# Kernel tuning notes

Measured on AMD Instinct MI355X. Metric: run time of the kernel, lower is better.

Reference implementation:

```python
import jax, jax.numpy as jnp
import numpy as np

N_HEAD = 16
D_HEAD = 64
HIDDEN = 1024
T = 2048
B = 4


def setup_inputs() -> dict:
    key = jax.random.key(0)
    k1, k2, k3, k4, k5 = jax.random.split(key, 5)
    qkv_out = (2 * N_HEAD + 1) * D_HEAD  # 2112
    return {
        "x": jax.random.normal(k1, (B, T, HIDDEN), dtype=jnp.float32),
        "w_qkv": jax.random.normal(k2, (qkv_out, HIDDEN), dtype=jnp.float32) * (HIDDEN ** -0.5),
        "b_qkv": jax.random.normal(k3, (qkv_out,), dtype=jnp.float32) * 0.02,
        "w_out": jax.random.normal(k4, (HIDDEN, D_HEAD), dtype=jnp.float32) * (D_HEAD ** -0.5),
        "b_out": jax.random.normal(k5, (HIDDEN,), dtype=jnp.float32) * 0.02,
    }


def reference(x, w_qkv, b_qkv, w_out, b_out):
    bs, t, h = x.shape
    scale = D_HEAD ** -0.5
    qkv = x @ w_qkv.T + b_qkv  # [b, t, (2H+1)*dh]
    q, k, v = jnp.split(qkv, [N_HEAD * D_HEAD, 2 * N_HEAD * D_HEAD], axis=-1)
    q = q.reshape(bs, t, N_HEAD, D_HEAD)
    k = k.reshape(bs, t, N_HEAD, D_HEAD)
    v = v.reshape(bs, t, D_HEAD)  # single V head shared across all heads
    # attn_score: [b, h, i, j]
    attn_score = jnp.einsum("bihd,bjhd->bhij", q, k) * scale
    # causal mask: -inf above diagonal
    causal = jnp.triu(jnp.full((t, t), -jnp.inf, dtype=attn_score.dtype), 1)
    attn_score = attn_score + causal
    attn_prob = jax.nn.softmax(attn_score, axis=-1)  # dropout is identity in eval
    # shared V across heads: [b,h,i,j] x [b,j,d] -> [b,h,i,d]
    attn_vec = jnp.einsum("bhij,bjd->bhid", attn_prob, v)
    m_attn_vec = jnp.mean(attn_vec, axis=1)  # mean over heads -> [b, t, d_head]
    out = m_attn_vec @ w_out.T + b_out  # [b, t, hidden]
    return out, attn_vec
```

## Files before the change

### kernel.cpp

```cpp
#include <hip/hip_runtime.h>
#include <hip/hip_bf16.h>
#include <math.h>

#define NHEAD 16
#define DHEAD 64
#define HIDDEN 1024
#define TSEQ 2048
#define BATCH 4
#define QKV_OUT 2112
#define BT (BATCH * TSEQ)

typedef __attribute__((ext_vector_type(8))) short bf16x8;
typedef __attribute__((ext_vector_type(4))) float floatx4;

static __device__ __forceinline__ short f2bf(float x) {
  __hip_bfloat16 h = __float2bfloat16(x);
  return *reinterpret_cast<short*>(&h);
}

#define MFMA16(a, b, c) __builtin_amdgcn_mfma_f32_16x16x32_bf16(a, b, c, 0, 0, 0)

__global__ __launch_bounds__(256) void f32_to_bf16(
    const float* __restrict__ src, short* __restrict__ dst, int n) {
  const int i = (blockIdx.x * 256 + threadIdx.x) * 8;
  if (i >= n) return;
  float4 a = *(const float4*)&src[i];
  float4 b = *(const float4*)&src[i + 4];
  short o[8];
  o[0] = f2bf(a.x); o[1] = f2bf(a.y); o[2] = f2bf(a.z); o[3] = f2bf(a.w);
  o[4] = f2bf(b.x); o[5] = f2bf(b.y); o[6] = f2bf(b.z); o[7] = f2bf(b.w);
  *(uint4*)&dst[i] = *(uint4*)o;
}

#define QK_BM 128
#define QK_BN 64
#define QK_BK 64

template <typename OUT_T>
__global__ __launch_bounds__(256) void gemm_mfma_bf16(
    const short* __restrict__ A, const short* __restrict__ B,
    const float* __restrict__ bias, OUT_T* __restrict__ C,
    int M, int N, int K) {
  __shared__ short As[QK_BM][72];
  __shared__ short Bs[QK_BN][72];

  const int tid = threadIdx.x;
  const int lane = tid & 63;
  const int wv = tid >> 6;
  const int ln = lane & 15;
  const int grp = lane >> 4;
  const int wm = wv >> 1;
  const int wn = wv & 1;
  const int rowbase = blockIdx.y * QK_BM;
  const int colbase = blockIdx.x * QK_BN;

  const int ar = tid >> 1, ac = (tid & 1) * 32;
  const int br = tid >> 2, bc = (tid & 3) * 16;

  floatx4 acc[4][2];
#pragma unroll
  for (int m = 0; m < 4; ++m)
#pragma unroll
    for (int n = 0; n < 2; ++n) acc[m][n] = (floatx4){0.f, 0.f, 0.f, 0.f};

  for (int k0 = 0; k0 < K; k0 += QK_BK) {
    const short* ap = A + (size_t)(rowbase + ar) * K + k0 + ac;
    uint4 a0 = *(const uint4*)(ap + 0);
    uint4 a1 = *(const uint4*)(ap + 8);
    uint4 a2 = *(const uint4*)(ap + 16);
    uint4 a3 = *(const uint4*)(ap + 24);
    const short* bp = B + (size_t)(colbase + br) * K + k0 + bc;
    uint4 b0 = *(const uint4*)(bp + 0);
    uint4 b1 = *(const uint4*)(bp + 8);
    __syncthreads();
    *(uint4*)&As[ar][ac + 0] = a0;
    *(uint4*)&As[ar][ac + 8] = a1;
    *(uint4*)&As[ar][ac + 16] = a2;
    *(uint4*)&As[ar][ac + 24] = a3;
    *(uint4*)&Bs[br][bc + 0] = b0;
    *(uint4*)&Bs[br][bc + 8] = b1;
    __syncthreads();

#pragma unroll
    for (int ks = 0; ks < 2; ++ks) {
      bf16x8 bfrag[2];
#pragma unroll
      for (int n = 0; n < 2; ++n)
        bfrag[n] = *(const bf16x8*)&Bs[wn * 32 + n * 16 + ln][ks * 32 + grp * 8];
#pragma unroll
      for (int m = 0; m < 4; ++m) {
        bf16x8 af = *(const bf16x8*)&As[wm * 64 + m * 16 + ln][ks * 32 + grp * 8];
#pragma unroll
        for (int n = 0; n < 2; ++n)
          acc[m][n] = MFMA16(af, bfrag[n], acc[m][n]);
      }
    }
  }

#pragma unroll
  for (int n = 0; n < 2; ++n) {
    const int col = colbase + wn * 32 + n * 16 + ln;
    const float bv = bias[col];
#pragma unroll
    for (int m = 0; m < 4; ++m) {
#pragma unroll
      for (int r = 0; r < 4; ++r) {
        const int row = rowbase + wm * 64 + m * 16 + grp * 4 + r;
        const float v = acc[m][n][r] + bv;
        if constexpr (sizeof(OUT_T) == 2)
          C[(size_t)row * N + col] = f2bf(v);
        else
          C[(size_t)row * N + col] = v;
      }
    }
  }
}

__global__ __launch_bounds__(256) void transpose_v(
    const short* __restrict__ qkv, short* __restrict__ vt) {
  __shared__ short tile[64][72];
  const int tt = blockIdx.x;
  const int b = blockIdx.y;
  const int tid = threadIdx.x;
  const int li = tid >> 2;
  const int lc = (tid & 3) * 16;

  const short* src = qkv + (size_t)(b * TSEQ + tt * 64 + li) * QKV_OUT + 2048 + lc;
  *(uint4*)&tile[li][lc] = *(const uint4*)src;
  *(uint4*)&tile[li][lc + 8] = *(const uint4*)(src + 8);
  __syncthreads();
  short tmp[16];
#pragma unroll
  for (int u = 0; u < 16; ++u) tmp[u] = tile[lc + u][li];
  short* dst = vt + (size_t)(b * 64 + li) * TSEQ + tt * 64 + lc;
  *(uint4*)dst = *(uint4*)&tmp[0];
  *(uint4*)(dst + 8) = *(uint4*)&tmp[8];
}

#define CH 8

__global__ __launch_bounds__(256) void attn_partial(
    const short* __restrict__ qkv, const short* __restrict__ vt,
    float* __restrict__ attn_vec, float* __restrict__ pO,
    float* __restrict__ pL) {
  __shared__ short Ks[64][72];
  __shared__ short Vt[64][72];
  __shared__ short Ps[64][72];

  const int x = gridDim.x - 1 - blockIdx.x;
  int it, jc;
  if (x < 8) {
    it = x; jc = 0;
  } else if (x < 24) {
    it = 8 + ((x - 8) >> 1); jc = (x - 8) & 1;
  } else if (x < 48) {
    it = 16 + (x - 24) / 3; jc = (x - 24) % 3;
  } else {
    it = 24 + ((x - 48) >> 2); jc = (x - 48) & 3;
  }
  const int jstart = jc * CH;
  const int jend = min(jstart + CH, it + 1);

  const int tid = threadIdx.x;
  const int h = blockIdx.y;
  const int b = blockIdx.z;
  const int lane = tid & 63;
  const int wv = tid >> 6;
  const int ln = lane & 15;
  const int grp = lane >> 4;
  const int qbase = wv * 16;
  const int sli = tid & 63;
  const int slc = (tid >> 6) * 16;
  const float CEXP = 0.18033688f;

  const short* qptr = qkv + (size_t)(b * TSEQ + it * 64 + qbase + ln) * QKV_OUT + h * 64;
  const bf16x8 bq0 = *(const bf16x8*)(qptr + grp * 8);
  const bf16x8 bq1 = *(const bf16x8*)(qptr + 32 + grp * 8);

  floatx4 oT[4];
#pragma unroll
  for (int m = 0; m < 4; ++m) oT[m] = (floatx4){0.f, 0.f, 0.f, 0.f};
  float lsum = 0.f;

  const short* ks0 = qkv + (size_t)(b * TSEQ + jstart * 64 + sli) * QKV_OUT + 1024 + h * 64 + slc;
  const short* vs0 = vt + (size_t)(b * 64 + sli) * TSEQ + jstart * 64 + slc;
  uint4 kr0 = *(const uint4*)ks0;
  uint4 kr1 = *(const uint4*)(ks0 + 8);
  uint4 vr0 = *(const uint4*)vs0;
  uint4 vr1 = *(const uint4*)(vs0 + 8);

  for (int jt = jstart; jt < jend; ++jt) {
    __syncthreads();
    *(uint4*)&Ks[sli][slc] = kr0;
    *(uint4*)&Ks[sli][slc + 8] = kr1;
    *(uint4*)&Vt[sli][slc] = vr0;
    *(uint4*)&Vt[sli][slc + 8] = vr1;
    __syncthreads();

    if (jt + 1 < jend) {
      const short* kn =
          qkv + (size_t)(b * TSEQ + (jt + 1) * 64 + sli) * QKV_OUT + 1024 + h * 64 + slc;
      const short* vn = vt + (size_t)(b * 64 + sli) * TSEQ + (jt + 1) * 64 + slc;
      kr0 = *(const uint4*)kn;
      kr1 = *(const uint4*)(kn + 8);
      vr0 = *(const uint4*)vn;
      vr1 = *(const uint4*)(vn + 8);
    }

    floatx4 st[4];
#pragma unroll
    for (int m = 0; m < 4; ++m) {
      bf16x8 ak0 = *(const bf16x8*)&Ks[m * 16 + ln][grp * 8];
      bf16x8 ak1 = *(const bf16x8*)&Ks[m * 16 + ln][32 + grp * 8];
      floatx4 a = (floatx4){0.f, 0.f, 0.f, 0.f};
      a = MFMA16(ak0, bq0, a);
      a = MFMA16(ak1, bq1, a);
      st[m] = a;
    }

    if (jt == it) {
#pragma unroll
      for (int m = 0; m < 4; ++m)
#pragma unroll
        for (int r = 0; r < 4; ++r)
          if (m * 16 + grp * 4 + r > qbase + ln) st[m][r] = -INFINITY;
    }

#pragma unroll
    for (int m = 0; m < 4; ++m) {
      float p0 = exp2f(CEXP * st[m][0]);
      float p1 = exp2f(CEXP * st[m][1]);
      float p2 = exp2f(CEXP * st[m][2]);
      float p3 = exp2f(CEXP * st[m][3]);
      lsum += (p0 + p1) + (p2 + p3);
      short pk[4] = {f2bf(p0), f2bf(p1), f2bf(p2), f2bf(p3)};
      *(uint2*)&Ps[qbase + ln][m * 16 + grp * 4] = *(uint2*)pk;
    }

    bf16x8 bp0 = *(const bf16x8*)&Ps[qbase + ln][grp * 8];
    bf16x8 bp1 = *(const bf16x8*)&Ps[qbase + ln][32 + grp * 8];
#pragma unroll
    for (int m = 0; m < 4; ++m) {
      bf16x8 av0 = *(const bf16x8*)&Vt[m * 16 + ln][grp * 8];
      bf16x8 av1 = *(const bf16x8*)&Vt[m * 16 + ln][32 + grp * 8];
      oT[m] = MFMA16(av0, bp0, oT[m]);
      oT[m] = MFMA16(av1, bp1, oT[m]);
    }
  }

  lsum += __shfl_xor(lsum, 16);
  lsum += __shfl_xor(lsum, 32);

  if (it < 8) {
    const float inv = 1.f / lsum;
    float* orow =
        attn_vec + ((size_t)(b * NHEAD + h) * TSEQ + it * 64 + qbase + ln) * DHEAD;
#pragma unroll
    for (int m = 0; m < 4; ++m) {
      float4 o4;
      o4.x = oT[m][0] * inv;
      o4.y = oT[m][1] * inv;
      o4.z = oT[m][2] * inv;
      o4.w = oT[m][3] * inv;
      *(float4*)&orow[m * 16 + grp * 4] = o4;
    }
  } else {
    const int slot = (it < 16) ? (it - 8) * 2 + jc
                   : (it < 24) ? 16 + (it - 16) * 3 + jc
                               : 40 + (it - 24) * 4 + jc;
    const size_t sbase = (size_t)(b * NHEAD + h) * 72 + slot;
    float* prow = pO + sbase * 4096 + (size_t)(qbase + ln) * 64;
#pragma unroll
    for (int m = 0; m < 4; ++m) {
      float4 o4;
      o4.x = oT[m][0]; o4.y = oT[m][1]; o4.z = oT[m][2]; o4.w = oT[m][3];
      *(float4*)&prow[m * 16 + grp * 4] = o4;
    }
    if (grp == 0) pL[sbase * 64 + qbase + ln] = lsum;
  }
}

__global__ __launch_bounds__(256) void attn_combine(
    const float* __restrict__ pO, const float* __restrict__ pL,
    float* __restrict__ attn_vec) {
  const int it = 8 + blockIdx.x;
  const int h = blockIdx.y;
  const int b = blockIdx.z;
  const int nch = (it < 16) ? 2 : (it < 24) ? 3 : 4;
  const int slot0 = (it < 16) ? (it - 8) * 2
                  : (it < 24) ? 16 + (it - 16) * 3
                              : 40 + (it - 24) * 4;
  const int q = threadIdx.x >> 2;
  const int dbase = (threadIdx.x & 3) * 16;
  const size_t base = (size_t)(b * NHEAD + h) * 72 + slot0;

  float4 acc[4];
#pragma unroll
  for (int u = 0; u < 4; ++u) acc[u] = (float4){0.f, 0.f, 0.f, 0.f};
  float l = 0.f;
  for (int c = 0; c < nch; ++c) {
    const float* pr = pO + (base + c) * 4096 + (size_t)q * 64 + dbase;
#pragma unroll
    for (int u = 0; u < 4; ++u) {
      float4 v = *(const float4*)&pr[u * 4];
      acc[u].x += v.x; acc[u].y += v.y; acc[u].z += v.z; acc[u].w += v.w;
    }
    l += pL[(base + c) * 64 + q];
  }
  const float inv = 1.f / l;
  float* orow =
      attn_vec + ((size_t)(b * NHEAD + h) * TSEQ + it * 64 + q) * DHEAD + dbase;
#pragma unroll
  for (int u = 0; u < 4; ++u) {
    float4 o4;
    o4.x = acc[u].x * inv; o4.y = acc[u].y * inv;
    o4.z = acc[u].z * inv; o4.w = acc[u].w * inv;
    *(float4*)&orow[u * 4] = o4;
  }
}

__global__ __launch_bounds__(256) void mean_heads(
    const float* __restrict__ attn_vec, short* __restrict__ m) {
  const int gid = blockIdx.x * 256 + threadIdx.x;
  const int d2 = (gid & 31) * 2;
  const int t = (gid >> 5) & (TSEQ - 1);
  const int b = gid >> 16;
  float s0 = 0.f, s1 = 0.f;
#pragma unroll
  for (int h = 0; h < NHEAD; ++h) {
    const float* p = &attn_vec[(((size_t)(b * NHEAD + h) * TSEQ) + t) * DHEAD + d2];
    s0 += p[0];
    s1 += p[1];
  }
  short pk[2] = {f2bf(s0 * (1.f / 16.f)), f2bf(s1 * (1.f / 16.f))};
  *(uint*)&m[gid * 2] = *(uint*)pk;
}

extern "C" void kernel_launch(void* const* d_in, const int* in_sizes, int n_in,
                              void* d_out, int out_size, void* d_ws, size_t ws_size,
                              hipStream_t stream) {
  const float* x     = (const float*)d_in[0];
  const float* w_qkv = (const float*)d_in[1];
  const float* b_qkv = (const float*)d_in[2];
  const float* w_out = (const float*)d_in[3];
  const float* b_out = (const float*)d_in[4];

  float* out      = (float*)d_out;
  float* attn_vec = out + (size_t)BT * HIDDEN;

  short* qkv_bf  = (short*)d_ws;
  short* vt_bf   = qkv_bf + (size_t)BT * QKV_OUT;
  short* wout_bf = vt_bf + (size_t)BATCH * DHEAD * TSEQ;
  short* m_attn  = wout_bf + (size_t)HIDDEN * DHEAD;
  char*  xbase   = (char*)(m_attn + (size_t)BT * DHEAD);
  short* x_bf    = (short*)xbase;
  short* w_bf    = x_bf + (size_t)BT * HIDDEN;
  float* pO      = (float*)xbase;
  float* pL      = pO + (size_t)64 * 72 * 4096;

  f32_to_bf16<<<dim3(BT * HIDDEN / 8 / 256), 256, 0, stream>>>(
      x, x_bf, BT * HIDDEN);
  f32_to_bf16<<<dim3(QKV_OUT * HIDDEN / 8 / 256), 256, 0, stream>>>(
      w_qkv, w_bf, QKV_OUT * HIDDEN);
  f32_to_bf16<<<dim3(HIDDEN * DHEAD / 8 / 256), 256, 0, stream>>>(
      w_out, wout_bf, HIDDEN * DHEAD);

  gemm_mfma_bf16<short><<<dim3(QKV_OUT / QK_BN, BT / QK_BM), 256, 0, stream>>>(
      x_bf, w_bf, b_qkv, qkv_bf, BT, QKV_OUT, HIDDEN);

  transpose_v<<<dim3(TSEQ / 64, BATCH), 256, 0, stream>>>(qkv_bf, vt_bf);

  attn_partial<<<dim3(80, NHEAD, BATCH), 256, 0, stream>>>(
      qkv_bf, vt_bf, attn_vec, pO, pL);

  attn_combine<<<dim3(24, NHEAD, BATCH), 256, 0, stream>>>(pO, pL, attn_vec);

  mean_heads<<<dim3(BT * DHEAD / 2 / 256), 256, 0, stream>>>(attn_vec, m_attn);

  gemm_mfma_bf16<float><<<dim3(HIDDEN / QK_BN, BT / QK_BM), 256, 0, stream>>>(
      m_attn, wout_bf, b_out, out, BT, HIDDEN, DHEAD);
}
```

Measured before the change: 285.4 us.

## Use direct global-to-LDS loads with 128x128 GEMM tiles; drop split-K attention

The GEMM now loads its tiles straight into shared memory through global_load_lds, using unpadded 128x128 tiles and clamping rows for the ragged N edge. This removes the register round trip and doubles per-block output reuse, at the cost of bank conflicts from the unpadded LDS layout. Attention goes back to one block per query tile covering the full causal range, which removes the partial-output buffers and the combine kernel. The price is a longer tail from the largest query tiles, since they are no longer split across blocks.

```diff
diff --git a/kernel.cpp b/kernel.cpp
--- a/kernel.cpp
+++ b/kernel.cpp
@@ -19,6 +19,12 @@
 }
 
 #define MFMA16(a, b, c) __builtin_amdgcn_mfma_f32_16x16x32_bf16(a, b, c, 0, 0, 0)
+
+static __device__ __forceinline__ void gload_lds16(const void* g, void* l) {
+  __builtin_amdgcn_global_load_lds(
+      (const __attribute__((address_space(1))) void*)g,
+      (__attribute__((address_space(3))) void*)l, 16, 0, 0);
+}
 
 __global__ __launch_bounds__(256) void f32_to_bf16(
     const float* __restrict__ src, short* __restrict__ dst, int n) {
@@ -32,17 +38,17 @@
   *(uint4*)&dst[i] = *(uint4*)o;
 }
 
-#define QK_BM 128
-#define QK_BN 64
-#define QK_BK 64
+#define GBM 128
+#define GBN 128
+#define GBK 64
 
 template <typename OUT_T>
-__global__ __launch_bounds__(256) void gemm_mfma_bf16(
+__global__ __launch_bounds__(256) void gemm_bt_gll(
     const short* __restrict__ A, const short* __restrict__ B,
     const float* __restrict__ bias, OUT_T* __restrict__ C,
     int M, int N, int K) {
-  __shared__ short As[QK_BM][72];
-  __shared__ short Bs[QK_BN][72];
+  __shared__ short As[GBM * GBK];
+  __shared__ short Bs[GBN * GBK];
 
   const int tid = threadIdx.x;
   const int lane = tid & 63;
@@ -51,66 +57,66 @@
   const int grp = lane >> 4;
   const int wm = wv >> 1;
   const int wn = wv & 1;
-  const int rowbase = blockIdx.y * QK_BM;
-  const int colbase = blockIdx.x * QK_BN;
-
-  const int ar = tid >> 1, ac = (tid & 1) * 32;
-  const int br = tid >> 2, bc = (tid & 3) * 16;
-
-  floatx4 acc[4][2];
+  const int rowbase = blockIdx.y * GBM;
+  const int colbase = blockIdx.x * GBN;
+
+  const int crow = lane >> 3;
+  const int kcol = (lane & 7) * 8;
+
+  floatx4 acc[4][4];
 #pragma unroll
   for (int m = 0; m < 4; ++m)
 #pragma unroll
-    for (int n = 0; n < 2; ++n) acc[m][n] = (floatx4){0.f, 0.f, 0.f, 0.f};
-
-  for (int k0 = 0; k0 < K; k0 += QK_BK) {
-    const short* ap = A + (size_t)(rowbase + ar) * K + k0 + ac;
-    uint4 a0 = *(const uint4*)(ap + 0);
-    uint4 a1 = *(const uint4*)(ap + 8);
-    uint4 a2 = *(const uint4*)(ap + 16);
-    uint4 a3 = *(const uint4*)(ap + 24);
-    const short* bp = B + (size_t)(colbase + br) * K + k0 + bc;
-    uint4 b0 = *(const uint4*)(bp + 0);
-    uint4 b1 = *(const uint4*)(bp + 8);
+    for (int n = 0; n < 4; ++n) acc[m][n] = (floatx4){0.f, 0.f, 0.f, 0.f};
+
+  for (int k0 = 0; k0 < K; k0 += GBK) {
     __syncthreads();
-    *(uint4*)&As[ar][ac + 0] = a0;
-    *(uint4*)&As[ar][ac + 8] = a1;
-    *(uint4*)&As[ar][ac + 16] = a2;
-    *(uint4*)&As[ar][ac + 24] = a3;
-    *(uint4*)&Bs[br][bc + 0] = b0;
-    *(uint4*)&Bs[br][bc + 8] = b1;
+#pragma unroll
+    for (int c = 0; c < 4; ++c) {
+      const int tr = (wv * 4 + c) * 8 + crow;
+      gload_lds16(A + (size_t)(rowbase + tr) * K + k0 + kcol,
+                  &As[(wv * 4 + c) * 8 * GBK]);
+      int br = colbase + tr;
+      if (br > N - 1) br = N - 1;
+      gload_lds16(B + (size_t)br * K + k0 + kcol,
+                  &Bs[(wv * 4 + c) * 8 * GBK]);
+    }
     __syncthreads();
 
 #pragma unroll
     for (int ks = 0; ks < 2; ++ks) {
-      bf16x8 bfrag[2];
-#pragma unroll
-      for (int n = 0; n < 2; ++n)
-        bfrag[n] = *(const bf16x8*)&Bs[wn * 32 + n * 16 + ln][ks * 32 + grp * 8];
+      bf16x8 bfrag[4];
+#pragma unroll
+      for (int n = 0; n < 4; ++n)
+        bfrag[n] =
+            *(const bf16x8*)&Bs[(wn * 64 + n * 16 + ln) * GBK + ks * 32 + grp * 8];
 #pragma unroll
       for (int m = 0; m < 4; ++m) {
-        bf16x8 af = *(const bf16x8*)&As[wm * 64 + m * 16 + ln][ks * 32 + grp * 8];
-#pragma unroll
-        for (int n = 0; n < 2; ++n)
+        bf16x8 af =
+            *(const bf16x8*)&As[(wm * 64 + m * 16 + ln) * GBK + ks * 32 + grp * 8];
+#pragma unroll
+        for (int n = 0; n < 4; ++n)
           acc[m][n] = MFMA16(af, bfrag[n], acc[m][n]);
       }
     }
   }
 
 #pragma unroll
-  for (int n = 0; n < 2; ++n) {
-    const int col = colbase + wn * 32 + n * 16 + ln;
-    const float bv = bias[col];
-#pragma unroll
-    for (int m = 0; m < 4; ++m) {
-#pragma unroll
-      for (int r = 0; r < 4; ++r) {
-        const int row = rowbase + wm * 64 + m * 16 + grp * 4 + r;
-        const float v = acc[m][n][r] + bv;
-        if constexpr (sizeof(OUT_T) == 2)
-          C[(size_t)row * N + col] = f2bf(v);
-        else
-          C[(size_t)row * N + col] = v;
+  for (int n = 0; n < 4; ++n) {
+    const int col = colbase + wn * 64 + n * 16 + ln;
+    if (col < N) {
+      const float bv = bias[col];
+#pragma unroll
+      for (int m = 0; m < 4; ++m) {
+#pragma unroll
+        for (int r = 0; r < 4; ++r) {
+          const int row = rowbase + wm * 64 + m * 16 + grp * 4 + r;
+          const float v = acc[m][n][r] + bv;
+          if constexpr (sizeof(OUT_T) == 2)
+            C[(size_t)row * N + col] = f2bf(v);
+          else
+            C[(size_t)row * N + col] = v;
+        }
       }
     }
   }
@@ -137,30 +143,14 @@
   *(uint4*)(dst + 8) = *(uint4*)&tmp[8];
 }
 
-#define CH 8
-
-__global__ __launch_bounds__(256) void attn_partial(
+__global__ __launch_bounds__(256) void attn_fused(
     const short* __restrict__ qkv, const short* __restrict__ vt,
-    float* __restrict__ attn_vec, float* __restrict__ pO,
-    float* __restrict__ pL) {
+    float* __restrict__ attn_vec) {
   __shared__ short Ks[64][72];
   __shared__ short Vt[64][72];
   __shared__ short Ps[64][72];
 
-  const int x = gridDim.x - 1 - blockIdx.x;
-  int it, jc;
-  if (x < 8) {
-    it = x; jc = 0;
-  } else if (x < 24) {
-    it = 8 + ((x - 8) >> 1); jc = (x - 8) & 1;
-  } else if (x < 48) {
-    it = 16 + (x - 24) / 3; jc = (x - 24) % 3;
-  } else {
-    it = 24 + ((x - 48) >> 2); jc = (x - 48) & 3;
-  }
-  const int jstart = jc * CH;
-  const int jend = min(jstart + CH, it + 1);
-
+  const int it = (int)gridDim.x - 1 - (int)blockIdx.x;
   const int tid = threadIdx.x;
   const int h = blockIdx.y;
   const int b = blockIdx.z;
@@ -182,14 +172,16 @@
   for (int m = 0; m < 4; ++m) oT[m] = (floatx4){0.f, 0.f, 0.f, 0.f};
   float lsum = 0.f;
 
-  const short* ks0 = qkv + (size_t)(b * TSEQ + jstart * 64 + sli) * QKV_OUT + 1024 + h * 64 + slc;
-  const short* vs0 = vt + (size_t)(b * 64 + sli) * TSEQ + jstart * 64 + slc;
+  const int jend = it + 1;
+
+  const short* ks0 = qkv + (size_t)(b * TSEQ + sli) * QKV_OUT + 1024 + h * 64 + slc;
+  const short* vs0 = vt + (size_t)(b * 64 + sli) * TSEQ + slc;
   uint4 kr0 = *(const uint4*)ks0;
   uint4 kr1 = *(const uint4*)(ks0 + 8);
   uint4 vr0 = *(const uint4*)vs0;
   uint4 vr1 = *(const uint4*)(vs0 + 8);
 
-  for (int jt = jstart; jt < jend; ++jt) {
+  for (int jt = 0; jt < jend; ++jt) {
     __syncthreads();
     *(uint4*)&Ks[sli][slc] = kr0;
     *(uint4*)&Ks[sli][slc + 8] = kr1;
@@ -251,71 +243,17 @@
   lsum += __shfl_xor(lsum, 16);
   lsum += __shfl_xor(lsum, 32);
 
-  if (it < 8) {
-    const float inv = 1.f / lsum;
-    float* orow =
-        attn_vec + ((size_t)(b * NHEAD + h) * TSEQ + it * 64 + qbase + ln) * DHEAD;
-#pragma unroll
-    for (int m = 0; m < 4; ++m) {
-      float4 o4;
-      o4.x = oT[m][0] * inv;
-      o4.y = oT[m][1] * inv;
-      o4.z = oT[m][2] * inv;
-      o4.w = oT[m][3] * inv;
-      *(float4*)&orow[m * 16 + grp * 4] = o4;
-    }
-  } else {
-    const int slot = (it < 16) ? (it - 8) * 2 + jc
-                   : (it < 24) ? 16 + (it - 16) * 3 + jc
-                               : 40 + (it - 24) * 4 + jc;
-    const size_t sbase = (size_t)(b * NHEAD + h) * 72 + slot;
-    float* prow = pO + sbase * 4096 + (size_t)(qbase + ln) * 64;
-#pragma unroll
-    for (int m = 0; m < 4; ++m) {
-      float4 o4;
-      o4.x = oT[m][0]; o4.y = oT[m][1]; o4.z = oT[m][2]; o4.w = oT[m][3];
-      *(float4*)&prow[m * 16 + grp * 4] = o4;
-    }
-    if (grp == 0) pL[sbase * 64 + qbase + ln] = lsum;
-  }
-}
-
-__global__ __launch_bounds__(256) void attn_combine(
-    const float* __restrict__ pO, const float* __restrict__ pL,
-    float* __restrict__ attn_vec) {
-  const int it = 8 + blockIdx.x;
-  const int h = blockIdx.y;
-  const int b = blockIdx.z;
-  const int nch = (it < 16) ? 2 : (it < 24) ? 3 : 4;
-  const int slot0 = (it < 16) ? (it - 8) * 2
-                  : (it < 24) ? 16 + (it - 16) * 3
-                              : 40 + (it - 24) * 4;
-  const int q = threadIdx.x >> 2;
-  const int dbase = (threadIdx.x & 3) * 16;
-  const size_t base = (size_t)(b * NHEAD + h) * 72 + slot0;
-
-  float4 acc[4];
-#pragma unroll
-  for (int u = 0; u < 4; ++u) acc[u] = (float4){0.f, 0.f, 0.f, 0.f};
-  float l = 0.f;
-  for (int c = 0; c < nch; ++c) {
-    const float* pr = pO + (base + c) * 4096 + (size_t)q * 64 + dbase;
-#pragma unroll
-    for (int u = 0; u < 4; ++u) {
-      float4 v = *(const float4*)&pr[u * 4];
-      acc[u].x += v.x; acc[u].y += v.y; acc[u].z += v.z; acc[u].w += v.w;
-    }
-    l += pL[(base + c) * 64 + q];
-  }
-  const float inv = 1.f / l;
+  const float inv = 1.f / lsum;
   float* orow =
-      attn_vec + ((size_t)(b * NHEAD + h) * TSEQ + it * 64 + q) * DHEAD + dbase;
-#pragma unroll
-  for (int u = 0; u < 4; ++u) {
+      attn_vec + ((size_t)(b * NHEAD + h) * TSEQ + it * 64 + qbase + ln) * DHEAD;
+#pragma unroll
+  for (int m = 0; m < 4; ++m) {
     float4 o4;
-    o4.x = acc[u].x * inv; o4.y = acc[u].y * inv;
-    o4.z = acc[u].z * inv; o4.w = acc[u].w * inv;
-    *(float4*)&orow[u * 4] = o4;
+    o4.x = oT[m][0] * inv;
+    o4.y = oT[m][1] * inv;
+    o4.z = oT[m][2] * inv;
+    o4.w = oT[m][3] * inv;
+    *(float4*)&orow[m * 16 + grp * 4] = o4;
   }
 }
 
@@ -352,11 +290,8 @@
   short* vt_bf   = qkv_bf + (size_t)BT * QKV_OUT;
   short* wout_bf = vt_bf + (size_t)BATCH * DHEAD * TSEQ;
   short* m_attn  = wout_bf + (size_t)HIDDEN * DHEAD;
-  char*  xbase   = (char*)(m_attn + (size_t)BT * DHEAD);
-  short* x_bf    = (short*)xbase;
+  short* x_bf    = m_attn + (size_t)BT * DHEAD;
   short* w_bf    = x_bf + (size_t)BT * HIDDEN;
-  float* pO      = (float*)xbase;
-  float* pL      = pO + (size_t)64 * 72 * 4096;
 
   f32_to_bf16<<<dim3(BT * HIDDEN / 8 / 256), 256, 0, stream>>>(
       x, x_bf, BT * HIDDEN);
@@ -365,18 +300,16 @@
   f32_to_bf16<<<dim3(HIDDEN * DHEAD / 8 / 256), 256, 0, stream>>>(
       w_out, wout_bf, HIDDEN * DHEAD);
 
-  gemm_mfma_bf16<short><<<dim3(QKV_OUT / QK_BN, BT / QK_BM), 256, 0, stream>>>(
+  gemm_bt_gll<short><<<dim3((QKV_OUT + GBN - 1) / GBN, BT / GBM), 256, 0, stream>>>(
       x_bf, w_bf, b_qkv, qkv_bf, BT, QKV_OUT, HIDDEN);
 
   transpose_v<<<dim3(TSEQ / 64, BATCH), 256, 0, stream>>>(qkv_bf, vt_bf);
 
-  attn_partial<<<dim3(80, NHEAD, BATCH), 256, 0, stream>>>(
-      qkv_bf, vt_bf, attn_vec, pO, pL);
-
-  attn_combine<<<dim3(24, NHEAD, BATCH), 256, 0, stream>>>(pO, pL, attn_vec);
+  attn_fused<<<dim3(TSEQ / 64, NHEAD, BATCH), 256, 0, stream>>>(
+      qkv_bf, vt_bf, attn_vec);
 
   mean_heads<<<dim3(BT * DHEAD / 2 / 256), 256, 0, stream>>>(attn_vec, m_attn);
 
-  gemm_mfma_bf16<float><<<dim3(HIDDEN / QK_BN, BT / QK_BM), 256, 0, stream>>>(
+  gemm_bt_gll<float><<<dim3(HIDDEN / GBN, BT / GBM), 256, 0, stream>>>(
       m_attn, wout_bf, b_out, out, BT, HIDDEN, DHEAD);
 }
```

Measured after the change: 329.7 us. 1.16x slower.

## Enlarge GEMM tile to 128x128 and prefetch next K-slab into registers

Applied to the files above, without the earlier changes.

The bf16 MFMA GEMM tile grows from 128x64 to 128x128, giving each wave a 64x64 output with 16 accumulators. This raises operand reuse per LDS load. Global loads for the next K step are now issued into registers before the MFMA loop, so memory latency can overlap compute. N edges are handled by clamping B rows and guarding column writes, because 2112 is not a multiple of 128. The larger tile leaves fewer blocks for the QKV GEMM, and the extra accumulators raise register pressure.

```diff
diff --git a/kernel.cpp b/kernel.cpp
--- a/kernel.cpp
+++ b/kernel.cpp
@@ -32,17 +32,17 @@
   *(uint4*)&dst[i] = *(uint4*)o;
 }
 
-#define QK_BM 128
-#define QK_BN 64
-#define QK_BK 64
+#define GBM 128
+#define GBN 128
+#define GBK 64
 
 template <typename OUT_T>
-__global__ __launch_bounds__(256) void gemm_mfma_bf16(
+__global__ __launch_bounds__(256) void gemm_bt(
     const short* __restrict__ A, const short* __restrict__ B,
     const float* __restrict__ bias, OUT_T* __restrict__ C,
     int M, int N, int K) {
-  __shared__ short As[QK_BM][72];
-  __shared__ short Bs[QK_BN][72];
+  __shared__ short As[GBM][72];
+  __shared__ short Bs[GBN][72];
 
   const int tid = threadIdx.x;
   const int lane = tid & 63;
@@ -51,66 +51,80 @@
   const int grp = lane >> 4;
   const int wm = wv >> 1;
   const int wn = wv & 1;
-  const int rowbase = blockIdx.y * QK_BM;
-  const int colbase = blockIdx.x * QK_BN;
-
-  const int ar = tid >> 1, ac = (tid & 1) * 32;
-  const int br = tid >> 2, bc = (tid & 3) * 16;
-
-  floatx4 acc[4][2];
+  const int rowbase = blockIdx.y * GBM;
+  const int colbase = blockIdx.x * GBN;
+
+  const int sr = tid >> 1;
+  const int sc = (tid & 1) * 32;
+  int brr = colbase + sr;
+  if (brr > N - 1) brr = N - 1;
+  const short* aptr = A + (size_t)(rowbase + sr) * K + sc;
+  const short* bptr = B + (size_t)brr * K + sc;
+
+  floatx4 acc[4][4];
 #pragma unroll
   for (int m = 0; m < 4; ++m)
 #pragma unroll
-    for (int n = 0; n < 2; ++n) acc[m][n] = (floatx4){0.f, 0.f, 0.f, 0.f};
-
-  for (int k0 = 0; k0 < K; k0 += QK_BK) {
-    const short* ap = A + (size_t)(rowbase + ar) * K + k0 + ac;
-    uint4 a0 = *(const uint4*)(ap + 0);
-    uint4 a1 = *(const uint4*)(ap + 8);
-    uint4 a2 = *(const uint4*)(ap + 16);
-    uint4 a3 = *(const uint4*)(ap + 24);
-    const short* bp = B + (size_t)(colbase + br) * K + k0 + bc;
-    uint4 b0 = *(const uint4*)(bp + 0);
-    uint4 b1 = *(const uint4*)(bp + 8);
+    for (int n = 0; n < 4; ++n) acc[m][n] = (floatx4){0.f, 0.f, 0.f, 0.f};
+
+  uint4 ar[4], brg[4];
+#pragma unroll
+  for (int c = 0; c < 4; ++c) {
+    ar[c] = *(const uint4*)(aptr + c * 8);
+    brg[c] = *(const uint4*)(bptr + c * 8);
+  }
+
+  for (int k0 = 0; k0 < K; k0 += GBK) {
     __syncthreads();
-    *(uint4*)&As[ar][ac + 0] = a0;
-    *(uint4*)&As[ar][ac + 8] = a1;
-    *(uint4*)&As[ar][ac + 16] = a2;
-    *(uint4*)&As[ar][ac + 24] = a3;
-    *(uint4*)&Bs[br][bc + 0] = b0;
-    *(uint4*)&Bs[br][bc + 8] = b1;
+#pragma unroll
+    for (int c = 0; c < 4; ++c) {
+      *(uint4*)&As[sr][sc + c * 8] = ar[c];
+      *(uint4*)&Bs[sr][sc + c * 8] = brg[c];
+    }
     __syncthreads();
 
+    if (k0 + GBK < K) {
+      aptr += GBK;
+      bptr += GBK;
+#pragma unroll
+      for (int c = 0; c < 4; ++c) {
+        ar[c] = *(const uint4*)(aptr + c * 8);
+        brg[c] = *(const uint4*)(bptr + c * 8);
+      }
+    }
+
 #pragma unroll
     for (int ks = 0; ks < 2; ++ks) {
-      bf16x8 bfrag[2];
-#pragma unroll
-      for (int n = 0; n < 2; ++n)
-        bfrag[n] = *(const bf16x8*)&Bs[wn * 32 + n * 16 + ln][ks * 32 + grp * 8];
+      bf16x8 bfrag[4];
+#pragma unroll
+      for (int n = 0; n < 4; ++n)
+        bfrag[n] = *(const bf16x8*)&Bs[wn * 64 + n * 16 + ln][ks * 32 + grp * 8];
 #pragma unroll
       for (int m = 0; m < 4; ++m) {
         bf16x8 af = *(const bf16x8*)&As[wm * 64 + m * 16 + ln][ks * 32 + grp * 8];
 #pragma unroll
-        for (int n = 0; n < 2; ++n)
+        for (int n = 0; n < 4; ++n)
           acc[m][n] = MFMA16(af, bfrag[n], acc[m][n]);
       }
     }
   }
 
 #pragma unroll
-  for (int n = 0; n < 2; ++n) {
-    const int col = colbase + wn * 32 + n * 16 + ln;
-    const float bv = bias[col];
-#pragma unroll
-    for (int m = 0; m < 4; ++m) {
-#pragma unroll
-      for (int r = 0; r < 4; ++r) {
-        const int row = rowbase + wm * 64 + m * 16 + grp * 4 + r;
-        const float v = acc[m][n][r] + bv;
-        if constexpr (sizeof(OUT_T) == 2)
-          C[(size_t)row * N + col] = f2bf(v);
-        else
-          C[(size_t)row * N + col] = v;
+  for (int n = 0; n < 4; ++n) {
+    const int col = colbase + wn * 64 + n * 16 + ln;
+    if (col < N) {
+      const float bv = bias[col];
+#pragma unroll
+      for (int m = 0; m < 4; ++m) {
+#pragma unroll
+        for (int r = 0; r < 4; ++r) {
+          const int row = rowbase + wm * 64 + m * 16 + grp * 4 + r;
+          const float v = acc[m][n][r] + bv;
+          if constexpr (sizeof(OUT_T) == 2)
+            C[(size_t)row * N + col] = f2bf(v);
+          else
+            C[(size_t)row * N + col] = v;
+        }
       }
     }
   }
@@ -365,7 +379,7 @@
   f32_to_bf16<<<dim3(HIDDEN * DHEAD / 8 / 256), 256, 0, stream>>>(
       w_out, wout_bf, HIDDEN * DHEAD);
 
-  gemm_mfma_bf16<short><<<dim3(QKV_OUT / QK_BN, BT / QK_BM), 256, 0, stream>>>(
+  gemm_bt<short><<<dim3((QKV_OUT + GBN - 1) / GBN, BT / GBM), 256, 0, stream>>>(
       x_bf, w_bf, b_qkv, qkv_bf, BT, QKV_OUT, HIDDEN);
 
   transpose_v<<<dim3(TSEQ / 64, BATCH), 256, 0, stream>>>(qkv_bf, vt_bf);
@@ -377,6 +391,6 @@
 
   mean_heads<<<dim3(BT * DHEAD / 2 / 256), 256, 0, stream>>>(attn_vec, m_attn);
 
-  gemm_mfma_bf16<float><<<dim3(HIDDEN / QK_BN, BT / QK_BM), 256, 0, stream>>>(
+  gemm_bt<float><<<dim3(HIDDEN / GBN, BT / GBM), 256, 0, stream>>>(
       m_attn, wout_bf, b_out, out, BT, HIDDEN, DHEAD);
 }
```

Measured after the change: 449.5 us. 1.58x slower.

## Load K and V MFMA operands directly from global memory, dropping LDS staging

Applied to the files above, without the earlier changes.

The attention kernel no longer stages K and V tiles through shared memory with a register prefetch and two block barriers per tile. Each wave now reads its MFMA operands straight from global memory (via L1/L2). This removes the LDS writes and the __syncthreads cost, but each of the 4 waves fetches the same K/V data redundantly and loses the software prefetch overlap, so load latency is exposed right before the MFMAs.

```diff
diff --git a/kernel.cpp b/kernel.cpp
--- a/kernel.cpp
+++ b/kernel.cpp
@@ -143,8 +143,6 @@
     const short* __restrict__ qkv, const short* __restrict__ vt,
     float* __restrict__ attn_vec, float* __restrict__ pO,
     float* __restrict__ pL) {
-  __shared__ short Ks[64][72];
-  __shared__ short Vt[64][72];
   __shared__ short Ps[64][72];
 
   const int x = gridDim.x - 1 - blockIdx.x;
@@ -169,49 +167,32 @@
   const int ln = lane & 15;
   const int grp = lane >> 4;
   const int qbase = wv * 16;
-  const int sli = tid & 63;
-  const int slc = (tid >> 6) * 16;
   const float CEXP = 0.18033688f;
 
   const short* qptr = qkv + (size_t)(b * TSEQ + it * 64 + qbase + ln) * QKV_OUT + h * 64;
   const bf16x8 bq0 = *(const bf16x8*)(qptr + grp * 8);
   const bf16x8 bq1 = *(const bf16x8*)(qptr + 32 + grp * 8);
 
+  const short* kb0 = qkv + (size_t)(b * TSEQ + jstart * 64 + 0) * QKV_OUT + 1024 +
+                     h * 64 + (size_t)ln * QKV_OUT + grp * 8;
+  const short* vb0 = vt + ((size_t)b * 64 + ln) * TSEQ + (size_t)jstart * 64 + grp * 8;
+  const size_t kmstep = (size_t)16 * QKV_OUT;
+  const size_t vmstep = (size_t)16 * TSEQ;
+
   floatx4 oT[4];
 #pragma unroll
   for (int m = 0; m < 4; ++m) oT[m] = (floatx4){0.f, 0.f, 0.f, 0.f};
   float lsum = 0.f;
 
-  const short* ks0 = qkv + (size_t)(b * TSEQ + jstart * 64 + sli) * QKV_OUT + 1024 + h * 64 + slc;
-  const short* vs0 = vt + (size_t)(b * 64 + sli) * TSEQ + jstart * 64 + slc;
-  uint4 kr0 = *(const uint4*)ks0;
-  uint4 kr1 = *(const uint4*)(ks0 + 8);
-  uint4 vr0 = *(const uint4*)vs0;
-  uint4 vr1 = *(const uint4*)(vs0 + 8);
-
   for (int jt = jstart; jt < jend; ++jt) {
-    __syncthreads();
-    *(uint4*)&Ks[sli][slc] = kr0;
-    *(uint4*)&Ks[sli][slc + 8] = kr1;
-    *(uint4*)&Vt[sli][slc] = vr0;
-    *(uint4*)&Vt[sli][slc + 8] = vr1;
-    __syncthreads();
-
-    if (jt + 1 < jend) {
-      const short* kn =
-          qkv + (size_t)(b * TSEQ + (jt + 1) * 64 + sli) * QKV_OUT + 1024 + h * 64 + slc;
-      const short* vn = vt + (size_t)(b * 64 + sli) * TSEQ + (jt + 1) * 64 + slc;
-      kr0 = *(const uint4*)kn;
-      kr1 = *(const uint4*)(kn + 8);
-      vr0 = *(const uint4*)vn;
-      vr1 = *(const uint4*)(vn + 8);
-    }
+    const short* kb = kb0 + (size_t)(jt - jstart) * 64 * QKV_OUT;
+    const short* vb = vb0 + (size_t)(jt - jstart) * 64;
 
     floatx4 st[4];
 #pragma unroll
     for (int m = 0; m < 4; ++m) {
-      bf16x8 ak0 = *(const bf16x8*)&Ks[m * 16 + ln][grp * 8];
-      bf16x8 ak1 = *(const bf16x8*)&Ks[m * 16 + ln][32 + grp * 8];
+      bf16x8 ak0 = *(const bf16x8*)(kb + m * kmstep);
+      bf16x8 ak1 = *(const bf16x8*)(kb + m * kmstep + 32);
       floatx4 a = (floatx4){0.f, 0.f, 0.f, 0.f};
       a = MFMA16(ak0, bq0, a);
       a = MFMA16(ak1, bq1, a);
@@ -241,8 +222,8 @@
     bf16x8 bp1 = *(const bf16x8*)&Ps[qbase + ln][32 + grp * 8];
 #pragma unroll
     for (int m = 0; m < 4; ++m) {
-      bf16x8 av0 = *(const bf16x8*)&Vt[m * 16 + ln][grp * 8];
-      bf16x8 av1 = *(const bf16x8*)&Vt[m * 16 + ln][32 + grp * 8];
+      bf16x8 av0 = *(const bf16x8*)(vb + m * vmstep);
+      bf16x8 av1 = *(const bf16x8*)(vb + m * vmstep + 32);
       oT[m] = MFMA16(av0, bp0, oT[m]);
       oT[m] = MFMA16(av1, bp1, oT[m]);
     }
```

Result: slower. 478.7 us (+67.7%).
